# Performance work log

Hardware: AMD Instinct MI355X
Metric: run time of the kernel (lower is better)

The kernel has to match this reference:

```python
import jax, jax.numpy as jnp
import numpy as np

# Model dims (match init_kwargs / input_specs)
B, L, D = 4, 1024, 512
CHI, S = 32, 4          # bond_dim, spatial_bond_dim
TRUNC_THR = 1e-4        # relative SVD truncation threshold
LN_EPS = 1e-6


def setup_inputs() -> dict:
    key = jax.random.key(0)
    ks = jax.random.split(key, 6)
    def dense(k, fi, fo):
        return jax.random.normal(k, (fi, fo), jnp.float32) / np.float32(np.sqrt(fi))
    return {
        "x": jax.random.normal(ks[0], (B, L, D), jnp.float32),
        "W_site": dense(ks[1], D, CHI * S * CHI),
        "b_site": jnp.zeros((CHI * S * CHI,), jnp.float32),
        "W_bridge": dense(ks[2], S * CHI, CHI),
        "b_bridge": jnp.zeros((CHI,), jnp.float32),
        "W_out": dense(ks[3], CHI, D),
        "b_out": jnp.zeros((D,), jnp.float32),
        "gamma": jnp.ones((D,), jnp.float32),
        "beta": jnp.zeros((D,), jnp.float32),
        "W_gate": dense(ks[4], D, D),
        "b_gate": jnp.zeros((D,), jnp.float32),
    }


def _mps_temporal_scan(x, site_weights):
    """Sequential O(L*chi^2) MPS scan with per-step SVD truncation.

    x: [B, L, D]; site_weights: [B, L, chi, s, chi].
    State h_t [B, chi] is the (normalized) left environment vector. Each step
    contracts the left vector (state + input injection from the first chi
    features, since initial_state is zeros) with the site tensor, truncates
    small singular values (relative threshold), and accumulates log-norms.
    Returns outputs [B, L, s*chi] and log_probs [B, L].
    """
    u_seq = jnp.transpose(x[:, :, :CHI], (1, 0, 2))            # [L, B, chi]
    A_seq = jnp.transpose(site_weights, (1, 0, 2, 3, 4))        # [L, B, chi, s, chi]

    def step(h, inp):
        A, u = inp                                              # [B,chi,s,chi], [B,chi]
        left = h + u                                            # input-driven left vector
        M = jnp.einsum('bl,blpr->bpr', left, A)                 # [B, s, chi]
        U, Sv, Vh = jnp.linalg.svd(M, full_matrices=False)      # Sv: [B, min(s,chi)]
        mask = (Sv >= TRUNC_THR * Sv[:, :1]).astype(M.dtype)    # relative truncation
        St = Sv * mask
        Mt = jnp.einsum('bik,bk,bkr->bir', U, St, Vh)           # truncated site matrix
        nrm = jnp.sqrt(jnp.sum(St * St, axis=-1) + 1e-12)       # Frobenius norm -> log prob
        v = jnp.sum(Mt, axis=1)                                 # contract physical index
        h_new = v / (jnp.linalg.norm(v, axis=-1, keepdims=True) + 1e-12)
        return h_new, (Mt.reshape(Mt.shape[0], -1), jnp.log(nrm))

    h0 = jnp.zeros((x.shape[0], CHI), x.dtype)                  # initial_state = zeros
    _, (outs, logp) = jax.lax.scan(step, h0, (A_seq, u_seq))
    return jnp.transpose(outs, (1, 0, 2)), jnp.transpose(logp, (1, 0))


def reference(x, W_site, b_site, W_bridge, b_bridge, W_out, b_out,
              gamma, beta, W_gate, b_gate):
    x = x.astype(jnp.float32)
    Bb, Ll = x.shape[0], x.shape[1]
    # site_tensor_proj: Dense(chi*s*chi) applied directly to inputs
    site_weights = (x @ W_site + b_site).reshape(Bb, Ll, CHI, S, CHI)
    outs, _logp = _mps_temporal_scan(x, site_weights)           # [B, L, s*chi]
    y = outs @ W_bridge + b_bridge                              # mps_bridge -> [B,L,chi]
    y = y @ W_out + b_out                                       # output_projection -> [B,L,D]
    # LayerNorm(eps=1e-6)
    mu = jnp.mean(y, axis=-1, keepdims=True)
    var = jnp.mean((y - mu) ** 2, axis=-1, keepdims=True)
    yn = (y - mu) * jax.lax.rsqrt(var + LN_EPS) * gamma + beta
    # gated residual
    gate = jax.nn.sigmoid(x @ W_gate + b_gate)
    return gate * yn + (1.0 - gate) * x
```

## Files before the change

### kernel.cpp

```cpp
#include <hip/hip_runtime.h>
#include <math.h>

#define B_   4
#define L_   1024
#define D_   512
#define CHI_ 32
#define S_   4
#define BT_  (B_ * L_)
#define NC_  2560
#define DPRE 8

__device__ __forceinline__ float readlane_f(float v, int l) {
    return __int_as_float(__builtin_amdgcn_readlane(__float_as_int(v), l));
}

__device__ __forceinline__ float bpermute_f(int byte_idx, float v) {
    return __int_as_float(__builtin_amdgcn_ds_bpermute(byte_idx, __float_as_int(v)));
}

template <int CTRL>
__device__ __forceinline__ float dpp_add(float x) {
    int y = __builtin_amdgcn_update_dpp(0, __float_as_int(x), CTRL, 0xf, 0xf, true);
    return x + __int_as_float(y);
}

__device__ __forceinline__ float reduce32_to_lane31(float x) {
    x = dpp_add<0x111>(x);
    x = dpp_add<0x112>(x);
    x = dpp_add<0x114>(x);
    x = dpp_add<0x118>(x);
    x = dpp_add<0x142>(x);
    return x;
}

__device__ __forceinline__ float octet_sum(float x) {
    x = dpp_add<0x111>(x);
    x = dpp_add<0x112>(x);
    x = dpp_add<0x114>(x);
    return x;
}

__global__ __launch_bounds__(256) void buildW_kernel(
    const float* __restrict__ Ws, const float* __restrict__ bs,
    const float* __restrict__ Wb, const float* __restrict__ Wg,
    const float* __restrict__ bg, float* __restrict__ Wcomb,
    float* __restrict__ biasC)
{
    const int tid = threadIdx.x;

    if (blockIdx.x == 512) {
        for (int f = tid; f < NC_; f += 256) {
            float acc;
            if (f < 1024) {
                const int q = f >> 8, rem = f & 255, i = rem >> 2, e = rem & 3;
                const int l = 4 * (i & 7) + e, r = (i >> 3) + 8 * q;
                const float* p = bs + l * 128 + r;
                acc = p[0] + p[32] + p[64] + p[96];
            } else if (f < 2048) {
                const int g = f - 1024, l = g >> 5, j = g & 31;
                acc = 0.f;
                for (int pr = 0; pr < 128; ++pr)
                    acc = fmaf(bs[l * 128 + pr], Wb[pr * 32 + j], acc);
            } else {
                acc = bg[f - 2048];
            }
            biasC[f] = acc;
        }
        return;
    }

    __shared__ float wsrow[4096];
    __shared__ float wbs[4096];

    const int d = blockIdx.x;
    #pragma unroll
    for (int i = 0; i < 16; ++i) {
        wsrow[i * 256 + tid] = Ws[(size_t)d * 4096 + i * 256 + tid];
        wbs[i * 256 + tid]   = Wb[i * 256 + tid];
    }
    __syncthreads();

    float* wrow = Wcomb + (size_t)d * NC_;

    #pragma unroll
    for (int ii = 0; ii < 4; ++ii) {
        const int f = ii * 256 + tid;
        const int q = f >> 8, rem = f & 255, i = rem >> 2, e = rem & 3;
        const int l = 4 * (i & 7) + e, r = (i >> 3) + 8 * q;
        const float* p = wsrow + l * 128 + r;
        wrow[f] = p[0] + p[32] + p[64] + p[96];
    }
    #pragma unroll
    for (int ii = 0; ii < 4; ++ii) {
        const int g = ii * 256 + tid;
        const int l = g >> 5, j = g & 31;
        float acc = 0.f;
        #pragma unroll 8
        for (int pr = 0; pr < 128; ++pr)
            acc = fmaf(wsrow[l * 128 + pr], wbs[pr * 32 + j], acc);
        wrow[1024 + g] = acc;
    }
    #pragma unroll
    for (int ii = 0; ii < 2; ++ii) {
        const int c = ii * 256 + tid;
        wrow[2048 + c] = Wg[(size_t)d * 512 + c];
    }
}

__global__ __launch_bounds__(256) void gemm_bias_kernel(
    const float* __restrict__ A, const float* __restrict__ Bm,
    const float* __restrict__ bias, float* __restrict__ C,
    int M, int N, int K)
{
    __shared__ float As[32][132];
    __shared__ float Bs[32][132];

    const int tid = threadIdx.x;
    const int tx = tid & 15;
    const int ty = tid >> 4;
    const int m0 = blockIdx.y * 128;
    const int n0 = blockIdx.x * 128;

    float acc[8][8] = {};

    for (int k0 = 0; k0 < K; k0 += 32) {
        #pragma unroll
        for (int p = 0; p < 4; ++p) {
            const int m = (tid >> 3) + 32 * p;
            const int k = (tid & 7) * 4;
            const float4 av = *(const float4*)(A + (size_t)(m0 + m) * K + k0 + k);
            As[k + 0][m] = av.x;
            As[k + 1][m] = av.y;
            As[k + 2][m] = av.z;
            As[k + 3][m] = av.w;
        }
        #pragma unroll
        for (int p = 0; p < 2; ++p) {
            const int k = (tid >> 4) + 16 * p;
            const int n = (tid & 15) * 8;
            const float* bp = Bm + (size_t)(k0 + k) * N + n0 + n;
            *(float4*)&Bs[k][n]     = *(const float4*)bp;
            *(float4*)&Bs[k][n + 4] = *(const float4*)(bp + 4);
        }
        __syncthreads();

        #pragma unroll
        for (int kk = 0; kk < 32; ++kk) {
            const float4 a0 = *(const float4*)&As[kk][ty * 8];
            const float4 a1 = *(const float4*)&As[kk][ty * 8 + 4];
            const float4 b0 = *(const float4*)&Bs[kk][tx * 8];
            const float4 b1 = *(const float4*)&Bs[kk][tx * 8 + 4];
            const float a[8] = {a0.x, a0.y, a0.z, a0.w, a1.x, a1.y, a1.z, a1.w};
            const float b[8] = {b0.x, b0.y, b0.z, b0.w, b1.x, b1.y, b1.z, b1.w};
            #pragma unroll
            for (int i = 0; i < 8; ++i)
                #pragma unroll
                for (int j = 0; j < 8; ++j)
                    acc[i][j] = fmaf(a[i], b[j], acc[i][j]);
        }
        __syncthreads();
    }

    const float4 bv0 = *(const float4*)&bias[n0 + tx * 8];
    const float4 bv1 = *(const float4*)&bias[n0 + tx * 8 + 4];
    #pragma unroll
    for (int i = 0; i < 8; ++i) {
        float* cp = C + (size_t)(m0 + ty * 8 + i) * N + n0 + tx * 8;
        float4 o0, o1;
        o0.x = acc[i][0] + bv0.x; o0.y = acc[i][1] + bv0.y;
        o0.z = acc[i][2] + bv0.z; o0.w = acc[i][3] + bv0.w;
        o1.x = acc[i][4] + bv1.x; o1.y = acc[i][5] + bv1.y;
        o1.z = acc[i][6] + bv1.z; o1.w = acc[i][7] + bv1.w;
        *(float4*)cp       = o0;
        *(float4*)(cp + 4) = o1;
    }
}

__global__ __launch_bounds__(256) void cvec_kernel(
    const float* __restrict__ Cc, const float* __restrict__ x,
    float* __restrict__ cBuf)
{
    const int tid  = threadIdx.x;
    const int lane = tid & 63;
    const int bt   = blockIdx.x * 4 + (tid >> 6);

    const float* base = Cc + (size_t)bt * NC_ + 4 * lane;
    float4 a0 = *(const float4*)(base + 0);
    float4 a1 = *(const float4*)(base + 256);
    float4 a2 = *(const float4*)(base + 512);
    float4 a3 = *(const float4*)(base + 768);

    const float u = x[(size_t)bt * D_ + (lane & 31)];
    const int idx0 = 16 * (lane & 7);
    const float u0 = bpermute_f(idx0 + 0,  u);
    const float u1 = bpermute_f(idx0 + 4,  u);
    const float u2 = bpermute_f(idx0 + 8,  u);
    const float u3 = bpermute_f(idx0 + 12, u);

    float p0 = fmaf(u3, a0.w, fmaf(u2, a0.z, fmaf(u1, a0.y, u0 * a0.x)));
    float p1 = fmaf(u3, a1.w, fmaf(u2, a1.z, fmaf(u1, a1.y, u0 * a1.x)));
    float p2 = fmaf(u3, a2.w, fmaf(u2, a2.z, fmaf(u1, a2.y, u0 * a2.x)));
    float p3 = fmaf(u3, a3.w, fmaf(u2, a3.z, fmaf(u1, a3.y, u0 * a3.x)));

    p0 = octet_sum(p0); p1 = octet_sum(p1);
    p2 = octet_sum(p2); p3 = octet_sum(p3);

    if ((lane & 7) == 7) {
        const int k = lane >> 3;
        float* cp = cBuf + (size_t)bt * 32 + k;
        cp[0]  = p0;
        cp[8]  = p1;
        cp[16] = p2;
        cp[24] = p3;
    }
}

__global__ __launch_bounds__(64, 1) void scan_kernel(
    const float* __restrict__ Cc, const float* __restrict__ cBuf,
    float* __restrict__ wOut)
{
    const int b   = blockIdx.x;
    const int tid = threadIdx.x;

    const float* At = Cc + (size_t)b * L_ * NC_ + 4 * tid;
    const float* cb = cBuf + (size_t)b * L_ * 32 + (tid & 31);
    float*       wo = wOut + (size_t)b * L_ * 64 + tid;

    const int idx0 = 16 * (tid & 7);
    const int idxR = 32 * (tid & 7) + 28;
    const bool selA = (tid >> 3) & 1;
    const bool selB = (tid >> 4) & 1;

    float4 areg[DPRE][4];
    float  creg[DPRE];

    #pragma unroll
    for (int j = 0; j < DPRE; ++j) {
        const float* ap = At + (size_t)j * NC_;
        #pragma unroll
        for (int q = 0; q < 4; ++q) areg[j][q] = *(const float4*)(ap + 256 * q);
        creg[j] = cb[j * 32];
    }

    float w = 0.f;

    for (int t = 0; t < L_; t += DPRE) {
        #pragma unroll
        for (int j = 0; j < DPRE; ++j) {
            wo[(t + j) * 64] = w;

            float red = reduce32_to_lane31(w * w);

            const float wb0 = bpermute_f(idx0 + 0,  w);
            const float wb1 = bpermute_f(idx0 + 4,  w);
            const float wb2 = bpermute_f(idx0 + 8,  w);
            const float wb3 = bpermute_f(idx0 + 12, w);

            float p0, p1, p2, p3;
            {
                const float4 a0 = areg[j][0], a1 = areg[j][1];
                const float4 a2 = areg[j][2], a3 = areg[j][3];
                p0 = fmaf(wb3, a0.w, fmaf(wb2, a0.z, fmaf(wb1, a0.y, wb0 * a0.x)));
                p1 = fmaf(wb3, a1.w, fmaf(wb2, a1.z, fmaf(wb1, a1.y, wb0 * a1.x)));
                p2 = fmaf(wb3, a2.w, fmaf(wb2, a2.z, fmaf(wb1, a2.y, wb0 * a2.x)));
                p3 = fmaf(wb3, a3.w, fmaf(wb2, a3.z, fmaf(wb1, a3.y, wb0 * a3.x)));
            }

            p0 = octet_sum(p0);
            p1 = octet_sum(p1);
            p2 = octet_sum(p2);
            p3 = octet_sum(p3);

            const float m0 = bpermute_f(idxR, p0);
            const float m1 = bpermute_f(idxR, p1);
            const float m2 = bpermute_f(idxR, p2);
            const float m3 = bpermute_f(idxR, p3);
            const float t0 = selA ? m1 : m0;
            const float t1 = selA ? m3 : m2;
            const float m  = selB ? t1 : t0;

            const float n2 = readlane_f(red, 31);
            const float rn = rsqrtf(n2 + 1e-24f);
            w = fmaf(m, rn, creg[j]);

            int tn = t + j + DPRE;
            if (tn > L_ - 1) tn = L_ - 1;
            const float* ap = At + (size_t)tn * NC_;
            #pragma unroll
            for (int q = 0; q < 4; ++q) areg[j][q] = *(const float4*)(ap + 256 * q);
            creg[j] = cb[tn * 32];
        }
    }
}

__global__ __launch_bounds__(128) void phaseB_kernel(
    const float* __restrict__ Cc, const float* __restrict__ x,
    const float* __restrict__ wBuf, const float* __restrict__ bb,
    float* __restrict__ y1)
{
    __shared__ float lf[32];
    __shared__ float part[4][32];

    const int bt = blockIdx.x;
    const int tid = threadIdx.x;

    if (tid < 64) {
        const float wv = wBuf[(size_t)bt * 64 + tid];
        float red = reduce32_to_lane31(wv * wv);
        const float n2 = readlane_f(red, 31);
        const float rn = rsqrtf(n2 + 1e-24f);
        if (tid < 32)
            lf[tid] = fmaf(wv, rn, x[(size_t)bt * D_ + tid]);
    }
    __syncthreads();

    const int j = tid & 31, q = tid >> 5;
    const float* Gp = Cc + (size_t)bt * NC_ + 1024;
    float p = 0.f;
    #pragma unroll
    for (int i = 0; i < 8; ++i)
        p = fmaf(lf[8 * q + i], Gp[(8 * q + i) * 32 + j], p);
    part[q][j] = p;
    __syncthreads();

    if (tid < 32)
        y1[bt * 32 + tid] = part[0][tid] + part[1][tid] + part[2][tid]
                          + part[3][tid] + bb[tid];
}

__global__ __launch_bounds__(256) void epilogue_kernel(
    const float* __restrict__ x, const float* __restrict__ y1buf,
    const float* __restrict__ Wout, const float* __restrict__ bout,
    const float* __restrict__ gamma, const float* __restrict__ beta,
    const float* __restrict__ Cc, float* __restrict__ out)
{
    __shared__ float ys[32];
    __shared__ float red1[4], red2[4];

    const int bt = blockIdx.x;
    const int tid = threadIdx.x;

    if (tid < 32) ys[tid] = y1buf[bt * 32 + tid];
    __syncthreads();

    float yv[2];
    #pragma unroll
    for (int q = 0; q < 2; ++q) {
        const int d = tid + q * 256;
        float acc = bout[d];
        #pragma unroll
        for (int j = 0; j < 32; ++j)
            acc = fmaf(ys[j], Wout[j * D_ + d], acc);
        yv[q] = acc;
    }

    float s1 = yv[0] + yv[1];
    float s2 = yv[0] * yv[0] + yv[1] * yv[1];
    #pragma unroll
    for (int m = 1; m <= 32; m <<= 1) {
        s1 += __shfl_xor(s1, m);
        s2 += __shfl_xor(s2, m);
    }
    const int wid = tid >> 6;
    if ((tid & 63) == 0) { red1[wid] = s1; red2[wid] = s2; }
    __syncthreads();
    const float S1 = red1[0] + red1[1] + red1[2] + red1[3];
    const float S2 = red2[0] + red2[1] + red2[2] + red2[3];
    const float mu  = S1 * (1.f / (float)D_);
    const float var = S2 * (1.f / (float)D_) - mu * mu;
    const float rstd = rsqrtf(var + 1e-6f);

    #pragma unroll
    for (int q = 0; q < 2; ++q) {
        const int d = tid + q * 256;
        const size_t gi = (size_t)bt * D_ + d;
        const float yn = (yv[q] - mu) * rstd * gamma[d] + beta[d];
        const float z = Cc[(size_t)bt * NC_ + 2048 + d];
        const float g = 1.f / (1.f + expf(-z));
        const float xv = x[gi];
        out[gi] = g * yn + (1.f - g) * xv;
    }
}

extern "C" void kernel_launch(void* const* d_in, const int* in_sizes, int n_in,
                              void* d_out, int out_size, void* d_ws, size_t ws_size,
                              hipStream_t stream)
{
    const float* x        = (const float*)d_in[0];
    const float* W_site   = (const float*)d_in[1];
    const float* b_site   = (const float*)d_in[2];
    const float* W_bridge = (const float*)d_in[3];
    const float* b_bridge = (const float*)d_in[4];
    const float* W_out    = (const float*)d_in[5];
    const float* b_out    = (const float*)d_in[6];
    const float* gamma    = (const float*)d_in[7];
    const float* beta     = (const float*)d_in[8];
    const float* W_gate   = (const float*)d_in[9];
    const float* b_gate   = (const float*)d_in[10];
    float* out = (float*)d_out;

    float* ws = (float*)d_ws;
    float* Wcomb = ws;
    float* biasC = Wcomb + (size_t)512 * NC_;
    float* Cc    = biasC + NC_;
    float* cBuf  = Cc    + (size_t)BT_ * NC_;
    float* wBuf  = cBuf  + (size_t)BT_ * 32;
    float* y1    = wBuf  + (size_t)BT_ * 64;

    buildW_kernel<<<dim3(513), dim3(256), 0, stream>>>(
        W_site, b_site, W_bridge, W_gate, b_gate, Wcomb, biasC);

    gemm_bias_kernel<<<dim3(NC_ / 128, BT_ / 128), dim3(256), 0, stream>>>(
        x, Wcomb, biasC, Cc, BT_, NC_, D_);

    cvec_kernel<<<dim3(BT_ / 4), dim3(256), 0, stream>>>(Cc, x, cBuf);

    scan_kernel<<<dim3(B_), dim3(64), 0, stream>>>(Cc, cBuf, wBuf);

    phaseB_kernel<<<dim3(BT_), dim3(128), 0, stream>>>(
        Cc, x, wBuf, b_bridge, y1);

    epilogue_kernel<<<dim3(BT_), dim3(256), 0, stream>>>(
        x, y1, W_out, b_out, gamma, beta, Cc, out);
}
```

Baseline: 455.0 us.

## Overlap latency-bound scan with remaining GEMM columns in a fused kernel

Splits the big GEMM so only the first 1024 output columns, which the scan and cvec need, are computed up front. The remaining 1536 columns are computed by extra blocks of a new fused kernel whose first four blocks run the sequential scan, so the GEMM work fills otherwise idle CUs during the scan. The risk is that GEMM blocks contend for memory bandwidth with the latency-sensitive scan, and the scan blocks now carry 256-thread launch bounds and shared memory.

```diff
diff --git a/kernel.cpp b/kernel.cpp
--- a/kernel.cpp
+++ b/kernel.cpp
@@ -107,19 +107,15 @@
     }
 }
 
-__global__ __launch_bounds__(256) void gemm_bias_kernel(
+__device__ __forceinline__ void gemm_tile_body(
     const float* __restrict__ A, const float* __restrict__ Bm,
     const float* __restrict__ bias, float* __restrict__ C,
-    int M, int N, int K)
-{
-    __shared__ float As[32][132];
-    __shared__ float Bs[32][132];
-
+    int M, int N, int K, int m0, int n0,
+    float (*As)[132], float (*Bs)[132])
+{
     const int tid = threadIdx.x;
     const int tx = tid & 15;
     const int ty = tid >> 4;
-    const int m0 = blockIdx.y * 128;
-    const int n0 = blockIdx.x * 128;
 
     float acc[8][8] = {};
 
@@ -176,6 +172,17 @@
     }
 }
 
+__global__ __launch_bounds__(256) void gemm_bias_kernel(
+    const float* __restrict__ A, const float* __restrict__ Bm,
+    const float* __restrict__ bias, float* __restrict__ C,
+    int M, int N, int K)
+{
+    __shared__ float As[32][132];
+    __shared__ float Bs[32][132];
+    gemm_tile_body(A, Bm, bias, C, M, N, K,
+                   blockIdx.y * 128, blockIdx.x * 128, As, Bs);
+}
+
 __global__ __launch_bounds__(256) void cvec_kernel(
     const float* __restrict__ Cc, const float* __restrict__ x,
     float* __restrict__ cBuf)
@@ -215,82 +222,95 @@
     }
 }
 
-__global__ __launch_bounds__(64, 1) void scan_kernel(
-    const float* __restrict__ Cc, const float* __restrict__ cBuf,
-    float* __restrict__ wOut)
-{
-    const int b   = blockIdx.x;
-    const int tid = threadIdx.x;
-
-    const float* At = Cc + (size_t)b * L_ * NC_ + 4 * tid;
-    const float* cb = cBuf + (size_t)b * L_ * 32 + (tid & 31);
-    float*       wo = wOut + (size_t)b * L_ * 64 + tid;
-
-    const int idx0 = 16 * (tid & 7);
-    const int idxR = 32 * (tid & 7) + 28;
-    const bool selA = (tid >> 3) & 1;
-    const bool selB = (tid >> 4) & 1;
-
-    float4 areg[DPRE][4];
-    float  creg[DPRE];
-
-    #pragma unroll
-    for (int j = 0; j < DPRE; ++j) {
-        const float* ap = At + (size_t)j * NC_;
-        #pragma unroll
-        for (int q = 0; q < 4; ++q) areg[j][q] = *(const float4*)(ap + 256 * q);
-        creg[j] = cb[j * 32];
-    }
-
-    float w = 0.f;
-
-    for (int t = 0; t < L_; t += DPRE) {
+__global__ __launch_bounds__(256) void fused_scan_gemm2_kernel(
+    const float* __restrict__ x, const float* __restrict__ Wcomb,
+    const float* __restrict__ biasC, float* __restrict__ Cc,
+    const float* __restrict__ cBuf, float* __restrict__ wOut)
+{
+    __shared__ float As[32][132];
+    __shared__ float Bs[32][132];
+
+    if (blockIdx.x < 4) {
+        const int tid = threadIdx.x;
+        if (tid >= 64) return;
+        const int b = blockIdx.x;
+
+        const float* At = Cc + (size_t)b * L_ * NC_ + 4 * tid;
+        const float* cb = cBuf + (size_t)b * L_ * 32 + (tid & 31);
+        float*       wo = wOut + (size_t)b * L_ * 64 + tid;
+
+        const int idx0 = 16 * (tid & 7);
+        const int idxR = 32 * (tid & 7) + 28;
+        const bool selA = (tid >> 3) & 1;
+        const bool selB = (tid >> 4) & 1;
+
+        float4 areg[DPRE][4];
+        float  creg[DPRE];
+
         #pragma unroll
         for (int j = 0; j < DPRE; ++j) {
-            wo[(t + j) * 64] = w;
-
-            float red = reduce32_to_lane31(w * w);
-
-            const float wb0 = bpermute_f(idx0 + 0,  w);
-            const float wb1 = bpermute_f(idx0 + 4,  w);
-            const float wb2 = bpermute_f(idx0 + 8,  w);
-            const float wb3 = bpermute_f(idx0 + 12, w);
-
-            float p0, p1, p2, p3;
-            {
-                const float4 a0 = areg[j][0], a1 = areg[j][1];
-                const float4 a2 = areg[j][2], a3 = areg[j][3];
-                p0 = fmaf(wb3, a0.w, fmaf(wb2, a0.z, fmaf(wb1, a0.y, wb0 * a0.x)));
-                p1 = fmaf(wb3, a1.w, fmaf(wb2, a1.z, fmaf(wb1, a1.y, wb0 * a1.x)));
-                p2 = fmaf(wb3, a2.w, fmaf(wb2, a2.z, fmaf(wb1, a2.y, wb0 * a2.x)));
-                p3 = fmaf(wb3, a3.w, fmaf(wb2, a3.z, fmaf(wb1, a3.y, wb0 * a3.x)));
-            }
-
-            p0 = octet_sum(p0);
-            p1 = octet_sum(p1);
-            p2 = octet_sum(p2);
-            p3 = octet_sum(p3);
-
-            const float m0 = bpermute_f(idxR, p0);
-            const float m1 = bpermute_f(idxR, p1);
-            const float m2 = bpermute_f(idxR, p2);
-            const float m3 = bpermute_f(idxR, p3);
-            const float t0 = selA ? m1 : m0;
-            const float t1 = selA ? m3 : m2;
-            const float m  = selB ? t1 : t0;
-
-            const float n2 = readlane_f(red, 31);
-            const float rn = rsqrtf(n2 + 1e-24f);
-            w = fmaf(m, rn, creg[j]);
-
-            int tn = t + j + DPRE;
-            if (tn > L_ - 1) tn = L_ - 1;
-            const float* ap = At + (size_t)tn * NC_;
+            const float* ap = At + (size_t)j * NC_;
             #pragma unroll
             for (int q = 0; q < 4; ++q) areg[j][q] = *(const float4*)(ap + 256 * q);
-            creg[j] = cb[tn * 32];
-        }
-    }
+            creg[j] = cb[j * 32];
+        }
+
+        float w = 0.f;
+
+        for (int t = 0; t < L_; t += DPRE) {
+            #pragma unroll
+            for (int j = 0; j < DPRE; ++j) {
+                wo[(t + j) * 64] = w;
+
+                float red = reduce32_to_lane31(w * w);
+
+                const float wb0 = bpermute_f(idx0 + 0,  w);
+                const float wb1 = bpermute_f(idx0 + 4,  w);
+                const float wb2 = bpermute_f(idx0 + 8,  w);
+                const float wb3 = bpermute_f(idx0 + 12, w);
+
+                float p0, p1, p2, p3;
+                {
+                    const float4 a0 = areg[j][0], a1 = areg[j][1];
+                    const float4 a2 = areg[j][2], a3 = areg[j][3];
+                    p0 = fmaf(wb3, a0.w, fmaf(wb2, a0.z, fmaf(wb1, a0.y, wb0 * a0.x)));
+                    p1 = fmaf(wb3, a1.w, fmaf(wb2, a1.z, fmaf(wb1, a1.y, wb0 * a1.x)));
+                    p2 = fmaf(wb3, a2.w, fmaf(wb2, a2.z, fmaf(wb1, a2.y, wb0 * a2.x)));
+                    p3 = fmaf(wb3, a3.w, fmaf(wb2, a3.z, fmaf(wb1, a3.y, wb0 * a3.x)));
+                }
+
+                p0 = octet_sum(p0);
+                p1 = octet_sum(p1);
+                p2 = octet_sum(p2);
+                p3 = octet_sum(p3);
+
+                const float m0 = bpermute_f(idxR, p0);
+                const float m1 = bpermute_f(idxR, p1);
+                const float m2 = bpermute_f(idxR, p2);
+                const float m3 = bpermute_f(idxR, p3);
+                const float t0 = selA ? m1 : m0;
+                const float t1 = selA ? m3 : m2;
+                const float m  = selB ? t1 : t0;
+
+                const float n2 = readlane_f(red, 31);
+                const float rn = rsqrtf(n2 + 1e-24f);
+                w = fmaf(m, rn, creg[j]);
+
+                int tn = t + j + DPRE;
+                if (tn > L_ - 1) tn = L_ - 1;
+                const float* ap = At + (size_t)tn * NC_;
+                #pragma unroll
+                for (int q = 0; q < 4; ++q) areg[j][q] = *(const float4*)(ap + 256 * q);
+                creg[j] = cb[tn * 32];
+            }
+        }
+        return;
+    }
+
+    const int g  = blockIdx.x - 4;
+    const int m0 = (g / 12) * 128;
+    const int n0 = 1024 + (g % 12) * 128;
+    gemm_tile_body(x, Wcomb, biasC, Cc, BT_, NC_, D_, m0, n0, As, Bs);
 }
 
 __global__ __launch_bounds__(128) void phaseB_kernel(
@@ -410,12 +430,13 @@
     buildW_kernel<<<dim3(513), dim3(256), 0, stream>>>(
         W_site, b_site, W_bridge, W_gate, b_gate, Wcomb, biasC);
 
-    gemm_bias_kernel<<<dim3(NC_ / 128, BT_ / 128), dim3(256), 0, stream>>>(
+    gemm_bias_kernel<<<dim3(8, BT_ / 128), dim3(256), 0, stream>>>(
         x, Wcomb, biasC, Cc, BT_, NC_, D_);
 
     cvec_kernel<<<dim3(BT_ / 4), dim3(256), 0, stream>>>(Cc, x, cBuf);
 
-    scan_kernel<<<dim3(B_), dim3(64), 0, stream>>>(Cc, cBuf, wBuf);
+    fused_scan_gemm2_kernel<<<dim3(4 + 12 * (BT_ / 128)), dim3(256), 0, stream>>>(
+        x, Wcomb, biasC, Cc, cBuf, wBuf);
 
     phaseB_kernel<<<dim3(BT_), dim3(128), 0, stream>>>(
         Cc, x, wBuf, b_bridge, y1);
```

After: 390.7 us. 1.16x faster.
